# Kernel tuning notes

Hardware: AMD Instinct MI355X
Metric: run time of the kernel (lower is better)

## Reference

```python
import jax, jax.numpy as jnp
import numpy as np

B, S, T = 256, 1024, 64  # batch, seq_len, num_tags


def setup_inputs() -> dict:
    key = jax.random.key(0)
    k1, k2, k3 = jax.random.split(key, 3)
    emissions = jax.random.normal(k1, (B, S, T), dtype=jnp.float32)
    tags = jax.random.randint(k2, (B, S), 0, T)
    mask = jnp.ones((B, S), dtype=bool)
    # nn.init.normal_(transitions, mean=0, std=0.1)
    transitions = 0.1 * jax.random.normal(k3, (T, T), dtype=jnp.float32)
    return {"emissions": emissions, "tags": tags, "mask": mask, "transitions": transitions}


def _crf_nll(emissions, transitions, tags, mask):
    maskf = mask.astype(emissions.dtype)
    # ---- gold score (_score_sentence) ----
    emit = jnp.take_along_axis(emissions, tags[..., None], axis=2)[..., 0]  # [B,S]
    emit_scores = (emit * maskf).sum(axis=1)
    trans_scores = (transitions[tags[:, :-1], tags[:, 1:]] * maskf[:, 1:]).sum(axis=1)
    gold = emit_scores + trans_scores  # [B]

    # ---- partition function (_forward_alg) via lax.scan ----
    alpha0 = emissions[:, 0]                      # [B,T]
    em_t = jnp.swapaxes(emissions[:, 1:], 0, 1)   # [S-1,B,T] time-major
    mk_t = jnp.swapaxes(mask[:, 1:], 0, 1)        # [S-1,B]

    def step(alpha, xs):
        e, m = xs
        # scores[b,i,j] = alpha[b,i] + trans[i,j] + emit[b,j]
        scores = alpha[:, :, None] + transitions[None, :, :] + e[:, None, :]
        new_alpha = jax.nn.logsumexp(scores, axis=1)  # [B,T]
        return jnp.where(m[:, None], new_alpha, alpha), None

    alpha, _ = jax.lax.scan(step, alpha0, (em_t, mk_t))
    fwd_score = jax.nn.logsumexp(alpha, axis=1)  # [B]

    # reduction='mean'
    return (fwd_score - gold).mean()


def reference(emissions, tags, mask, transitions):
    return _crf_nll(emissions, transitions, tags, mask)
```

## Files before the change

### kernel.cpp

```cpp
#include <hip/hip_runtime.h>
#include <hip/hip_bf16.h>
#include <cstdint>
#include <cstddef>


#define BB 256
#define SS 1024
#define TT 64
#define LN2f 0.69314718055994530942f
#define VF 272
#define VB 271
#define MMs 60
#define MSB 273

typedef _Float16 h2  __attribute__((ext_vector_type(2)));
typedef _Float16 h8  __attribute__((ext_vector_type(8)));
typedef float    f32x16 __attribute__((ext_vector_type(16)));
typedef int      i4v __attribute__((ext_vector_type(4)));

__device__ __forceinline__ float wred(float v) {
#pragma unroll
    for (int m = 32; m; m >>= 1) v += __shfl_xor(v, m, 64);
    return v;
}

__device__ __forceinline__ float rescale(float qn, int& kacc) {
    int bq = __builtin_amdgcn_readfirstlane(__float_as_int(qn));
    int k  = ((bq >> 23) & 255) - 127;
    kacc += k;
    return qn * __int_as_float((127 - k) << 23);
}

__device__ __forceinline__ float matvec64(float bc, const h2* Epk) {
    int nq = __builtin_amdgcn_mov_dpp(__float_as_int(bc), 0xB1, 0xF, 0xF, true);
    int pki = __builtin_bit_cast(int,
                  __builtin_amdgcn_cvt_pkrtz(bc, __int_as_float(nq)));
    int sp[32];
#pragma unroll
    for (int p = 0; p < 32; ++p)
        sp[p] = __builtin_amdgcn_readlane(pki, 2 * p);
    float a0 = 0.f, a1 = 0.f, a2 = 0.f, a3 = 0.f;
#pragma unroll
    for (int p = 0; p < 32; p += 4) {
        a0 = __builtin_amdgcn_fdot2(__builtin_bit_cast(h2, sp[p + 0]), Epk[p + 0], a0, false);
        a1 = __builtin_amdgcn_fdot2(__builtin_bit_cast(h2, sp[p + 1]), Epk[p + 1], a1, false);
        a2 = __builtin_amdgcn_fdot2(__builtin_bit_cast(h2, sp[p + 2]), Epk[p + 2], a2, false);
        a3 = __builtin_amdgcn_fdot2(__builtin_bit_cast(h2, sp[p + 3]), Epk[p + 3], a3, false);
    }
    return (a0 + a1) + (a2 + a3);
}

#define VSTEPF(EVAL)                                                       \
    {                                                                      \
        float ee = __expf(EVAL);                                           \
        float t  = matvec64(state, Epk);                                   \
        state    = rescale(t * ee, kacc);                                  \
    }
#define VSTEPB(EVAL)                                                       \
    {                                                                      \
        float ee = __expf(EVAL);                                           \
        float t  = matvec64(state * ee, Epk);                              \
        state    = rescale(t, kacc);                                       \
    }

#define PKRTZ(a, b) __builtin_bit_cast(int, __builtin_amdgcn_cvt_pkrtz((a), (b)))
#define SWAP32(x, y) asm("v_permlane32_swap_b32 %0, %1" : "+v"(x), "+v"(y))

#define CONV(CC, OUTA, OUTB)                                               \
    {                                                                      \
        int p0 = PKRTZ(CC[0], CC[1]);   int p1 = PKRTZ(CC[2], CC[3]);      \
        int p2 = PKRTZ(CC[4], CC[5]);   int p3 = PKRTZ(CC[6], CC[7]);      \
        SWAP32(p0, p2);  SWAP32(p1, p3);                                   \
        i4v da = {p0, p1, p2, p3};                                         \
        OUTA = __builtin_bit_cast(h8, da);                                 \
        int q0 = PKRTZ(CC[8], CC[9]);   int q1 = PKRTZ(CC[10], CC[11]);    \
        int q2 = PKRTZ(CC[12], CC[13]); int q3 = PKRTZ(CC[14], CC[15]);    \
        SWAP32(q0, q2);  SWAP32(q1, q3);                                   \
        i4v db = {q0, q1, q2, q3};                                         \
        OUTB = __builtin_bit_cast(h8, db);                                 \
    }

__device__ __forceinline__ f32x16 zz16() {
    f32x16 z;
#pragma unroll
    for (int q = 0; q < 16; ++q) z[q] = 0.f;
    return z;
}

#define MSTEP(MB, MINV, KACC, KLAST, E0V, E1V)                             \
    {                                                                      \
        float ee0 = __expf(E0V), ee1 = __expf(E1V);                        \
        float m0f = ee0 * MINV, m1f = ee1 * MINV;                          \
        h2 mp0 = __builtin_bit_cast(h2, __builtin_amdgcn_cvt_pkrtz(m0f, m0f)); \
        h2 mp1 = __builtin_bit_cast(h2, __builtin_amdgcn_cvt_pkrtz(m1f, m1f)); \
        h8 ms0 = __builtin_shufflevector(mp0, mp0, 0,1,0,1,0,1,0,1);       \
        h8 ms1 = __builtin_shufflevector(mp1, mp1, 0,1,0,1,0,1,0,1);       \
        h8 A0[4], A1[4];                                                   \
        _Pragma("unroll")                                                  \
        for (int kk = 0; kk < 4; ++kk) { A0[kk] = EfT[0][kk] * ms0;        \
                                         A1[kk] = EfT[1][kk] * ms1; }      \
        f32x16 c00 = __builtin_amdgcn_mfma_f32_32x32x16_f16(A0[0], MB[0][0], CZ, 0, 0, 0); \
        f32x16 c01 = __builtin_amdgcn_mfma_f32_32x32x16_f16(A0[0], MB[1][0], CZ, 0, 0, 0); \
        f32x16 c10 = __builtin_amdgcn_mfma_f32_32x32x16_f16(A1[0], MB[0][0], CZ, 0, 0, 0); \
        f32x16 c11 = __builtin_amdgcn_mfma_f32_32x32x16_f16(A1[0], MB[1][0], CZ, 0, 0, 0); \
        _Pragma("unroll")                                                  \
        for (int kk = 1; kk < 4; ++kk) {                                   \
            c00 = __builtin_amdgcn_mfma_f32_32x32x16_f16(A0[kk], MB[0][kk], c00, 0, 0, 0); \
            c01 = __builtin_amdgcn_mfma_f32_32x32x16_f16(A0[kk], MB[1][kk], c01, 0, 0, 0); \
            c10 = __builtin_amdgcn_mfma_f32_32x32x16_f16(A1[kk], MB[0][kk], c10, 0, 0, 0); \
            c11 = __builtin_amdgcn_mfma_f32_32x32x16_f16(A1[kk], MB[1][kk], c11, 0, 0, 0); \
        }                                                                  \
        int bq = __builtin_amdgcn_readfirstlane(__float_as_int(c00[0]));   \
        int k  = ((bq >> 23) & 255) - 127;                                 \
        KACC += k;  KLAST = k;                                             \
        MINV = __int_as_float((127 - k) << 23);                            \
        CONV(c00, MB[0][0], MB[0][1]);                                     \
        CONV(c10, MB[0][2], MB[0][3]);                                     \
        CONV(c01, MB[1][0], MB[1][1]);                                     \
        CONV(c11, MB[1][2], MB[1][3]);                                     \
    }

__global__ __launch_bounds__(384) void crf_fwd_kernel(
    const float* __restrict__ emissions,
    const int*   __restrict__ tags,
    const float* __restrict__ trans,
    float*       __restrict__ ws)
{
    const int b   = blockIdx.x;
    const int tid = threadIdx.x;
    const int w   = tid >> 6;
    const int j   = tid & 63;
    const float* em = emissions + (size_t)b * (SS * TT);
    const int*   tg = tags + b * SS;

    __shared__ float shq[TT];
    __shared__ float shu[TT];
    __shared__ float shg[2];
    __shared__ int   shkk[10];
    __shared__ int   shkr;

    if (tid == 0) shkr = 0;

    const bool isMat = (w == 0) || (w == 1) || (w == 4) || (w == 5);
    const int  widx  = (w < 2) ? w : (w - 2);
    const int  hh    = j >> 5;
    const int  cc_   = j & 31;

    h8 MbA[2][4], MbB[2][4];

    if (w == 2 || w == 3) {
        int t0v[8], t1v[8];
#pragma unroll
        for (int c = 0; c < 8; ++c) {
            int s = ((w - 2) * 8 + c) * TT + j;
            t0v[c] = tg[s];
            t1v[c] = tg[(s < SS - 1) ? s + 1 : s];
        }

        h2 Epk[32];
        float state;
        int  kacc = 0;
        float ge[8], gt[8];

        if (w == 2) {
#pragma unroll
            for (int p = 0; p < 32; ++p) {
                float x = __expf(trans[(2 * p + 0) * TT + j]);
                float y = __expf(trans[(2 * p + 1) * TT + j]);
                Epk[p] = __builtin_bit_cast(h2, __builtin_amdgcn_cvt_pkrtz(x, y));
            }
            state = __expf(em[j]);
            float eb[8];
#pragma unroll
            for (int u = 0; u < 8; ++u) eb[u] = em[(1 + u) * TT + j];
#pragma unroll
            for (int c = 0; c < 8; ++c) {
                int s = (0 * 8 + c) * TT + j;
                ge[c] = em[s * TT + t0v[c]];
                gt[c] = trans[t0v[c] * TT + t1v[c]];
            }
            for (int s0 = 1; s0 < 1 + VF; s0 += 8) {
                float en[8];
#pragma unroll
                for (int u = 0; u < 8; ++u)
                    en[u] = em[(s0 + 8 + u) * TT + j];
#pragma unroll
                for (int u = 0; u < 8; ++u) VSTEPF(eb[u]);
#pragma unroll
                for (int u = 0; u < 8; ++u) eb[u] = en[u];
            }
            shq[j] = state;
        } else {
#pragma unroll
            for (int p = 0; p < 32; ++p) {
                float x = __expf(trans[j * TT + 2 * p + 0]);
                float y = __expf(trans[j * TT + 2 * p + 1]);
                Epk[p] = __builtin_bit_cast(h2, __builtin_amdgcn_cvt_pkrtz(x, y));
            }
            state = 1.0f;
            float ep[7], eb[8];
#pragma unroll
            for (int u = 0; u < 7; ++u) ep[u] = em[(1023 - u) * TT + j];
#pragma unroll
            for (int u = 0; u < 8; ++u) eb[u] = em[(1016 - u) * TT + j];
#pragma unroll
            for (int c = 0; c < 8; ++c) {
                int s = (8 + c) * TT + j;
                ge[c] = em[s * TT + t0v[c]];
                float tr = trans[t0v[c] * TT + t1v[c]];
                gt[c] = (s == SS - 1) ? 0.f : tr;
            }
#pragma unroll
            for (int u = 0; u < 7; ++u) VSTEPB(ep[u]);
            for (int t0 = 0; t0 < VB - 7; t0 += 8) {
                float en[8];
#pragma unroll
                for (int u = 0; u < 8; ++u)
                    en[u] = em[(1016 - (t0 + 8 + u)) * TT + j];
#pragma unroll
                for (int u = 0; u < 8; ++u) VSTEPB(eb[u]);
#pragma unroll
                for (int u = 0; u < 8; ++u) eb[u] = en[u];
            }
            shu[j] = state;
        }

        float g = 0.f;
#pragma unroll
        for (int c = 0; c < 8; ++c) g += ge[c] + gt[c];
        g = wred(g);
        if (j == 0) { shg[w - 2] = g; shkk[8 + (w - 2)] = kacc; }
    } else {
        const int sA = MSB + MMs * (2 * widx);
        const int sB = sA + MMs;

        h8 EfT[2][4];
#pragma unroll
        for (int rr = 0; rr < 2; ++rr)
#pragma unroll
            for (int kk = 0; kk < 4; ++kk) {
                h8 v;
#pragma unroll
                for (int e = 0; e < 8; ++e)
                    v[e] = (_Float16)__expf(trans[(16 * kk + 8 * hh + e) * TT + 32 * rr + cc_]);
                EfT[rr][kk] = v;
            }
#pragma unroll
        for (int gg = 0; gg < 2; ++gg)
#pragma unroll
            for (int kk = 0; kk < 4; ++kk) {
                h8 v;
#pragma unroll
                for (int e = 0; e < 8; ++e)
                    v[e] = (_Float16)((16 * kk + 8 * hh + e == 32 * gg + cc_) ? 1.0f : 0.0f);
                MbA[gg][kk] = v;
                MbB[gg][kk] = v;
            }

        const f32x16 CZ = zz16();
        float minvA = 1.0f, minvB = 1.0f;
        int   kaccA = 0, kaccB = 0, klastA = 0, klastB = 0;
        float ebA0[4], ebA1[4], ebB0[4], ebB1[4];
#pragma unroll
        for (int u = 0; u < 4; ++u) {
            ebA0[u] = em[(sA + u) * TT + cc_];
            ebA1[u] = em[(sA + u) * TT + 32 + cc_];
            ebB0[u] = em[(sB + u) * TT + cc_];
            ebB1[u] = em[(sB + u) * TT + 32 + cc_];
        }

        for (int s0 = 0; s0 < MMs; s0 += 4) {
            float enA0[4], enA1[4], enB0[4], enB1[4];
#pragma unroll
            for (int u = 0; u < 4; ++u) {
                enA0[u] = em[(sA + s0 + 4 + u) * TT + cc_];
                enA1[u] = em[(sA + s0 + 4 + u) * TT + 32 + cc_];
                enB0[u] = em[(sB + s0 + 4 + u) * TT + cc_];
                enB1[u] = em[(sB + s0 + 4 + u) * TT + 32 + cc_];
            }
#pragma unroll
            for (int u = 0; u < 4; ++u) {
                MSTEP(MbA, minvA, kaccA, klastA, ebA0[u], ebA1[u]);
                MSTEP(MbB, minvB, kaccB, klastB, ebB0[u], ebB1[u]);
            }
#pragma unroll
            for (int u = 0; u < 4; ++u) {
                ebA0[u] = enA0[u]; ebA1[u] = enA1[u];
                ebB0[u] = enB0[u]; ebB1[u] = enB1[u];
            }
        }
        if (j == 0) {
            shkk[2 * widx]     = kaccA - klastA;
            shkk[2 * widx + 1] = kaccB - klastB;
        }
    }

    __syncthreads();

#pragma unroll
    for (int m = 7; m >= 0; --m) {
        if (isMat && (m >> 1) == widx) {
            const bool useB = (m & 1) != 0;
            float p0 = 0.f, p1 = 0.f;
#pragma unroll
            for (int kk = 0; kk < 4; ++kk)
#pragma unroll
                for (int e = 0; e < 8; ++e) {
                    float uval = shu[16 * kk + 8 * hh + e];
                    _Float16 a0 = useB ? MbB[0][kk][e] : MbA[0][kk][e];
                    _Float16 a1 = useB ? MbB[1][kk][e] : MbA[1][kk][e];
                    p0 += (float)a0 * uval;
                    p1 += (float)a1 * uval;
                }
            p0 += __shfl_xor(p0, 32, 64);
            p1 += __shfl_xor(p1, 32, 64);
            int bu = __builtin_amdgcn_readfirstlane(__float_as_int(p0));
            int ku = ((bu >> 23) & 255) - 127;
            float sc = __int_as_float((127 - ku) << 23);
            shu[cc_]      = p0 * sc;
            shu[32 + cc_] = p1 * sc;
            if (j == 0) shkr += ku;
        }
        __syncthreads();
    }

    if (w == 2) {
        float pr  = shq[j] * shu[j];
        float sum = wred(pr);
        int ksum = shkr;
#pragma unroll
        for (int q = 0; q < 10; ++q) ksum += shkk[q];
        float fwd = __logf(sum) + (float)ksum * LN2f;
        if (j == 0) ws[b] = fwd - (shg[0] + shg[1]);
    }
}

__global__ __launch_bounds__(256) void crf_reduce_kernel(
    const float* __restrict__ ws, float* __restrict__ out)
{
    int t = threadIdx.x;
    float v = ws[t];
#pragma unroll
    for (int m = 32; m; m >>= 1) v += __shfl_xor(v, m, 64);
    __shared__ float sh[4];
    if ((t & 63) == 0) sh[t >> 6] = v;
    __syncthreads();
    if (t == 0) out[0] = (sh[0] + sh[1] + sh[2] + sh[3]) * (1.0f / BB);
}

extern "C" void kernel_launch(void* const* d_in, const int* in_sizes, int n_in,
                              void* d_out, int out_size, void* d_ws, size_t ws_size,
                              hipStream_t stream) {
    const float* emissions = (const float*)d_in[0];
    const int*   tags      = (const int*)d_in[1];
    const float* trans     = (const float*)d_in[3];
    float* ws = (float*)d_ws;

    crf_fwd_kernel<<<BB, 384, 0, stream>>>(emissions, tags, trans, ws);
    crf_reduce_kernel<<<1, BB, 0, stream>>>(ws, (float*)d_out);
}
```

Measured before the change: 176.1 us.

## Split matrix-chain MFMA step into column-group phases to cut register pressure

The per-step matrix product update now runs in two column-group phases, one per output half, and interleaves the A and B chains inside each phase. Only two accumulators per chain are live at a time instead of four, which lowers VGPR/AGPR pressure. The launch bounds now request two blocks per CU, and the emission prefetch depth drops from 4 to 2 steps. In exchange, less independent MFMA work is in flight per phase and emission loads have less time to hide latency. The scale factor is read before the second phase rewrites the matrix, so the result appears unchanged.

```diff
diff --git a/kernel.cpp b/kernel.cpp
--- a/kernel.cpp
+++ b/kernel.cpp
@@ -87,40 +87,55 @@
     return z;
 }
 
-#define MSTEP(MB, MINV, KACC, KLAST, E0V, E1V)                             \
+#define GPHASE(ACC0, ACC1, MS0, MS1, MBG)                                  \
+    ACC0 = __builtin_amdgcn_mfma_f32_32x32x16_f16(EfT[0][0] * MS0, MBG[0], CZ, 0, 0, 0); \
+    ACC1 = __builtin_amdgcn_mfma_f32_32x32x16_f16(EfT[1][0] * MS1, MBG[0], CZ, 0, 0, 0); \
+    _Pragma("unroll")                                                      \
+    for (int kk = 1; kk < 4; ++kk) {                                       \
+        ACC0 = __builtin_amdgcn_mfma_f32_32x32x16_f16(EfT[0][kk] * MS0, MBG[kk], ACC0, 0, 0, 0); \
+        ACC1 = __builtin_amdgcn_mfma_f32_32x32x16_f16(EfT[1][kk] * MS1, MBG[kk], ACC1, 0, 0, 0); \
+    }
+
+#define WINDOW(EA0V, EA1V, EB0V, EB1V)                                     \
     {                                                                      \
-        float ee0 = __expf(E0V), ee1 = __expf(E1V);                        \
-        float m0f = ee0 * MINV, m1f = ee1 * MINV;                          \
-        h2 mp0 = __builtin_bit_cast(h2, __builtin_amdgcn_cvt_pkrtz(m0f, m0f)); \
-        h2 mp1 = __builtin_bit_cast(h2, __builtin_amdgcn_cvt_pkrtz(m1f, m1f)); \
-        h8 ms0 = __builtin_shufflevector(mp0, mp0, 0,1,0,1,0,1,0,1);       \
-        h8 ms1 = __builtin_shufflevector(mp1, mp1, 0,1,0,1,0,1,0,1);       \
-        h8 A0[4], A1[4];                                                   \
-        _Pragma("unroll")                                                  \
-        for (int kk = 0; kk < 4; ++kk) { A0[kk] = EfT[0][kk] * ms0;        \
-                                         A1[kk] = EfT[1][kk] * ms1; }      \
-        f32x16 c00 = __builtin_amdgcn_mfma_f32_32x32x16_f16(A0[0], MB[0][0], CZ, 0, 0, 0); \
-        f32x16 c01 = __builtin_amdgcn_mfma_f32_32x32x16_f16(A0[0], MB[1][0], CZ, 0, 0, 0); \
-        f32x16 c10 = __builtin_amdgcn_mfma_f32_32x32x16_f16(A1[0], MB[0][0], CZ, 0, 0, 0); \
-        f32x16 c11 = __builtin_amdgcn_mfma_f32_32x32x16_f16(A1[0], MB[1][0], CZ, 0, 0, 0); \
-        _Pragma("unroll")                                                  \
-        for (int kk = 1; kk < 4; ++kk) {                                   \
-            c00 = __builtin_amdgcn_mfma_f32_32x32x16_f16(A0[kk], MB[0][kk], c00, 0, 0, 0); \
-            c01 = __builtin_amdgcn_mfma_f32_32x32x16_f16(A0[kk], MB[1][kk], c01, 0, 0, 0); \
-            c10 = __builtin_amdgcn_mfma_f32_32x32x16_f16(A1[kk], MB[0][kk], c10, 0, 0, 0); \
-            c11 = __builtin_amdgcn_mfma_f32_32x32x16_f16(A1[kk], MB[1][kk], c11, 0, 0, 0); \
+        float eA0 = __expf(EA0V) * minvA, eA1 = __expf(EA1V) * minvA;      \
+        float eB0 = __expf(EB0V) * minvB, eB1 = __expf(EB1V) * minvB;      \
+        h2 tA0 = __builtin_bit_cast(h2, __builtin_amdgcn_cvt_pkrtz(eA0, eA0)); \
+        h2 tA1 = __builtin_bit_cast(h2, __builtin_amdgcn_cvt_pkrtz(eA1, eA1)); \
+        h2 tB0 = __builtin_bit_cast(h2, __builtin_amdgcn_cvt_pkrtz(eB0, eB0)); \
+        h2 tB1 = __builtin_bit_cast(h2, __builtin_amdgcn_cvt_pkrtz(eB1, eB1)); \
+        h8 msA0 = __builtin_shufflevector(tA0, tA0, 0,1,0,1,0,1,0,1);      \
+        h8 msA1 = __builtin_shufflevector(tA1, tA1, 0,1,0,1,0,1,0,1);      \
+        h8 msB0 = __builtin_shufflevector(tB0, tB0, 0,1,0,1,0,1,0,1);      \
+        h8 msB1 = __builtin_shufflevector(tB1, tB1, 0,1,0,1,0,1,0,1);      \
+        f32x16 a0, a1, b0, b1;                                             \
+        GPHASE(a0, a1, msA0, msA1, MbA[0]);                                \
+        GPHASE(b0, b1, msB0, msB1, MbB[0]);                                \
+        {                                                                  \
+            int bq = __builtin_amdgcn_readfirstlane(__float_as_int(a0[0])); \
+            int k  = ((bq >> 23) & 255) - 127;                             \
+            kaccA += k;  klastA = k;                                       \
+            minvA = __int_as_float((127 - k) << 23);                       \
         }                                                                  \
-        int bq = __builtin_amdgcn_readfirstlane(__float_as_int(c00[0]));   \
-        int k  = ((bq >> 23) & 255) - 127;                                 \
-        KACC += k;  KLAST = k;                                             \
-        MINV = __int_as_float((127 - k) << 23);                            \
-        CONV(c00, MB[0][0], MB[0][1]);                                     \
-        CONV(c10, MB[0][2], MB[0][3]);                                     \
-        CONV(c01, MB[1][0], MB[1][1]);                                     \
-        CONV(c11, MB[1][2], MB[1][3]);                                     \
-    }
-
-__global__ __launch_bounds__(384) void crf_fwd_kernel(
+        CONV(a0, MbA[0][0], MbA[0][1]);                                    \
+        CONV(a1, MbA[0][2], MbA[0][3]);                                    \
+        {                                                                  \
+            int bq = __builtin_amdgcn_readfirstlane(__float_as_int(b0[0])); \
+            int k  = ((bq >> 23) & 255) - 127;                             \
+            kaccB += k;  klastB = k;                                       \
+            minvB = __int_as_float((127 - k) << 23);                       \
+        }                                                                  \
+        CONV(b0, MbB[0][0], MbB[0][1]);                                    \
+        CONV(b1, MbB[0][2], MbB[0][3]);                                    \
+        GPHASE(a0, a1, msA0, msA1, MbA[1]);                                \
+        GPHASE(b0, b1, msB0, msB1, MbB[1]);                                \
+        CONV(a0, MbA[1][0], MbA[1][1]);                                    \
+        CONV(a1, MbA[1][2], MbA[1][3]);                                    \
+        CONV(b0, MbB[1][0], MbB[1][1]);                                    \
+        CONV(b1, MbB[1][2], MbB[1][3]);                                    \
+    }
+
+__global__ __launch_bounds__(384, 2) void crf_fwd_kernel(
     const float* __restrict__ emissions,
     const int*   __restrict__ tags,
     const float* __restrict__ trans,
@@ -260,31 +275,28 @@
         const f32x16 CZ = zz16();
         float minvA = 1.0f, minvB = 1.0f;
         int   kaccA = 0, kaccB = 0, klastA = 0, klastB = 0;
-        float ebA0[4], ebA1[4], ebB0[4], ebB1[4];
-#pragma unroll
-        for (int u = 0; u < 4; ++u) {
+        float ebA0[2], ebA1[2], ebB0[2], ebB1[2];
+#pragma unroll
+        for (int u = 0; u < 2; ++u) {
             ebA0[u] = em[(sA + u) * TT + cc_];
             ebA1[u] = em[(sA + u) * TT + 32 + cc_];
             ebB0[u] = em[(sB + u) * TT + cc_];
             ebB1[u] = em[(sB + u) * TT + 32 + cc_];
         }
 
-        for (int s0 = 0; s0 < MMs; s0 += 4) {
-            float enA0[4], enA1[4], enB0[4], enB1[4];
-#pragma unroll
-            for (int u = 0; u < 4; ++u) {
-                enA0[u] = em[(sA + s0 + 4 + u) * TT + cc_];
-                enA1[u] = em[(sA + s0 + 4 + u) * TT + 32 + cc_];
-                enB0[u] = em[(sB + s0 + 4 + u) * TT + cc_];
-                enB1[u] = em[(sB + s0 + 4 + u) * TT + 32 + cc_];
-            }
-#pragma unroll
-            for (int u = 0; u < 4; ++u) {
-                MSTEP(MbA, minvA, kaccA, klastA, ebA0[u], ebA1[u]);
-                MSTEP(MbB, minvB, kaccB, klastB, ebB0[u], ebB1[u]);
-            }
-#pragma unroll
-            for (int u = 0; u < 4; ++u) {
+        for (int s0 = 0; s0 < MMs; s0 += 2) {
+            float enA0[2], enA1[2], enB0[2], enB1[2];
+#pragma unroll
+            for (int u = 0; u < 2; ++u) {
+                enA0[u] = em[(sA + s0 + 2 + u) * TT + cc_];
+                enA1[u] = em[(sA + s0 + 2 + u) * TT + 32 + cc_];
+                enB0[u] = em[(sB + s0 + 2 + u) * TT + cc_];
+                enB1[u] = em[(sB + s0 + 2 + u) * TT + 32 + cc_];
+            }
+            WINDOW(ebA0[0], ebA1[0], ebB0[0], ebB1[0]);
+            WINDOW(ebA0[1], ebA1[1], ebB0[1], ebB1[1]);
+#pragma unroll
+            for (int u = 0; u < 2; ++u) {
                 ebA0[u] = enA0[u]; ebA1[u] = enA1[u];
                 ebB0[u] = enB0[u]; ebB1[u] = enB1[u];
             }
```

After: 184.2 us. +4.6%, slower.
